# Optimization experiments

Hardware: AMD Instinct MI355X
Metric: run time of the kernel (lower is better)

Reference implementation:

```python
import jax, jax.numpy as jnp
import numpy as np

ATOM_FDIM = 133
BOND_FDIM = 147  # atom features (133) + bond features (14)
HIDDEN = 300
DEPTH = 3
N_ATOMS = 200_000
N_BONDS = 400_000
MAX_NB = 6
N_MOLS = 10_000


def setup_inputs() -> dict:
    key = jax.random.key(0)
    ks = jax.random.split(key, 10)
    f_atoms = jax.random.normal(ks[0], (N_ATOMS, ATOM_FDIM), jnp.float32)
    f_bonds = jax.random.normal(ks[1], (N_BONDS, BOND_FDIM), jnp.float32)
    a2b = jax.random.randint(ks[2], (N_ATOMS, MAX_NB), 0, N_BONDS)
    b2a = jax.random.randint(ks[3], (N_BONDS,), 0, N_ATOMS)
    b2revb = jax.random.randint(ks[4], (N_BONDS,), 0, N_BONDS)
    a2mol = jnp.sort(jax.random.randint(ks[5], (N_ATOMS,), 0, N_MOLS))
    # learned params (chemprop MPNEncoder: W_i/W_h bias=False, W_o bias=True)
    s_i = 1.0 / np.sqrt(BOND_FDIM)
    s_h = 1.0 / np.sqrt(HIDDEN)
    s_o = 1.0 / np.sqrt(ATOM_FDIM + HIDDEN)
    W_i = jax.random.uniform(ks[6], (BOND_FDIM, HIDDEN), jnp.float32, -s_i, s_i)
    W_h = jax.random.uniform(ks[7], (HIDDEN, HIDDEN), jnp.float32, -s_h, s_h)
    W_o = jax.random.uniform(ks[8], (ATOM_FDIM + HIDDEN, HIDDEN), jnp.float32, -s_o, s_o)
    b_o = jax.random.uniform(ks[9], (HIDDEN,), jnp.float32, -s_o, s_o)
    return {"f_atoms": f_atoms, "f_bonds": f_bonds, "W_i": W_i, "W_h": W_h,
            "W_o": W_o, "b_o": b_o, "a2b": a2b, "b2a": b2a, "b2revb": b2revb,
            "a2mol": a2mol, "n_mols": N_MOLS}


def reference(f_atoms, f_bonds, W_i, W_h, W_o, b_o, a2b, b2a, b2revb, a2mol, n_mols):
    # input = W_i(f_bonds); message = ReLU(input)
    inp = f_bonds @ W_i                              # [n_bonds, H]
    message = jax.nn.relu(inp)
    for _ in range(DEPTH - 1):
        # gather incoming bond messages per atom and sum (index_select_ND + sum)
        a_message = message[a2b].sum(axis=1)         # [n_atoms, H]
        # message_b = a_message[b2a] - message[b2revb]
        new_msg = a_message[b2a] - message[b2revb]   # [n_bonds, H]
        message = jax.nn.relu(inp + new_msg @ W_h)
    # final atom hidden states
    a_message = message[a2b].sum(axis=1)             # [n_atoms, H]
    a_input = jnp.concatenate([f_atoms, a_message], axis=1)
    atom_hiddens = jax.nn.relu(a_input @ W_o + b_o)  # [n_atoms, H]
    # mean readout per molecule (scatter-sum / count)
    sums = jax.ops.segment_sum(atom_hiddens, a2mol, num_segments=n_mols)
    counts = jax.ops.segment_sum(jnp.ones((atom_hiddens.shape[0],), atom_hiddens.dtype),
                                 a2mol, num_segments=n_mols)
    mol_vecs = sums / jnp.maximum(counts, 1.0)[:, None]  # [n_mols, H]
    return mol_vecs
```

## Files before the change

### kernel.cpp

```cpp
#include <hip/hip_runtime.h>


#define HID 300
#define AFD 133
#define BFD 147
#define PAD 320

typedef _Float16 h16;
typedef _Float16 f16x8 __attribute__((ext_vector_type(8)));
typedef float    f32x4 __attribute__((ext_vector_type(4)));

__device__ __forceinline__ float relu_(float x) { return x > 0.f ? x : 0.f; }

union FragA { f16x8 v; h16 h[8]; uint4 u4; };
union H4    { uint2 u2; h16 h[4]; };

__global__ __launch_bounds__(256)
void pack_w(const float* __restrict__ Wa, const float* __restrict__ Wb,
            h16* __restrict__ dst, int KT, int mode)
{
    int e = blockIdx.x * 256 + threadIdx.x;
    if (e >= KT * 1280) return;
    int cc = e & 15, g = (e >> 4) & 3, p = (e >> 6) % 20, kt = e / 1280;
    int c = p * 16 + cc;
    FragA w;
    #pragma unroll
    for (int j = 0; j < 8; ++j) {
        int k = kt * 32 + g * 8 + j;
        float x = 0.f;
        if (c < HID) {
            if (mode == 0)      { if (k < BFD) x = Wa[k * HID + c]; }
            else if (mode == 1) { if (k < HID) x = Wa[k * HID + c];
                                  else if (k >= 320 && k < 467) x = Wb[(k - 320) * HID + c]; }
            else                { if (k < AFD) x = Wa[k * HID + c];
                                  else if (k >= 160 && k < 460) x = Wa[(k - 27) * HID + c]; }
        }
        w.h[j] = (h16)x;
    }
    *(uint4*)(dst + (size_t)e * 8) = w.u4;
}

template<int MODE>
__global__ __launch_bounds__(256)
void mgemm(const h16* __restrict__ G, const float* __restrict__ F,
           const h16* __restrict__ Wp, const float* __restrict__ bias,
           h16* __restrict__ outH, float* __restrict__ outF)
{
    constexpr int KT = (MODE == 0) ? 5 : 15;
    const int t  = threadIdx.x;
    const int l  = t & 63, wv = t >> 6;
    const int g  = l >> 4, cc = l & 15;
    const int m0 = blockIdx.x * 64;

    const h16*   pG[4];
    const float* pF[4];
    #pragma unroll
    for (int mt = 0; mt < 4; ++mt) {
        int r = m0 + mt * 16 + cc;
        if (MODE != 0) pG[mt] = G + (size_t)r * PAD + g * 8;
        pF[mt] = F + (size_t)r * ((MODE == 2) ? AFD : BFD);
    }
    const h16* pW = Wp + (size_t)(wv * 5) * 512 + g * 128 + cc * 8;

    f32x4 acc[4][5];
    #pragma unroll
    for (int mt = 0; mt < 4; ++mt)
        #pragma unroll
        for (int nt = 0; nt < 5; ++nt)
            acc[mt][nt] = (f32x4){0.f, 0.f, 0.f, 0.f};

    #pragma unroll
    for (int kt = 0; kt < KT; ++kt) {
        const int ks = kt * 32 + g * 8;
        FragA a[4];
        #pragma unroll
        for (int mt = 0; mt < 4; ++mt) {
            if (MODE == 0) {
                #pragma unroll
                for (int j = 0; j < 8; ++j) {
                    int kk = ks + j;
                    a[mt].h[j] = (h16)((kk < BFD) ? pF[mt][kk] : 0.f);
                }
            } else if (MODE == 1) {
                if (kt < 10) {
                    a[mt].u4 = *(const uint4*)(pG[mt] + kt * 32);
                } else {
                    #pragma unroll
                    for (int j = 0; j < 8; ++j) {
                        int kk = ks - 320 + j;
                        a[mt].h[j] = (h16)((kk < BFD) ? pF[mt][kk] : 0.f);
                    }
                }
            } else {
                if (kt < 5) {
                    #pragma unroll
                    for (int j = 0; j < 8; ++j) {
                        int kk = ks + j;
                        a[mt].h[j] = (h16)((kk < AFD) ? pF[mt][kk] : 0.f);
                    }
                } else {
                    a[mt].u4 = *(const uint4*)(pG[mt] + kt * 32 - 160);
                }
            }
        }
        f16x8 bf[5];
        #pragma unroll
        for (int nt = 0; nt < 5; ++nt)
            bf[nt] = *(const f16x8*)(pW + (size_t)kt * 10240 + nt * 512);
        #pragma unroll
        for (int mt = 0; mt < 4; ++mt)
            #pragma unroll
            for (int nt = 0; nt < 5; ++nt)
                acc[mt][nt] = __builtin_amdgcn_mfma_f32_16x16x32_f16(
                                  a[mt].v, bf[nt], acc[mt][nt], 0, 0, 0);
    }

    #pragma unroll
    for (int mt = 0; mt < 4; ++mt)
        #pragma unroll
        for (int nt = 0; nt < 5; ++nt) {
            int col = (wv * 5 + nt) * 16 + cc;
            float bb = 0.f;
            if (MODE == 2 && col < HID) bb = bias[col];
            #pragma unroll
            for (int rr = 0; rr < 4; ++rr) {
                int row = m0 + mt * 16 + g * 4 + rr;
                float v = relu_(acc[mt][nt][rr] + bb);
                if (MODE == 2) { if (col < HID) outF[(size_t)row * HID + col] = v; }
                else           outH[(size_t)row * PAD + col] = (h16)v;
            }
        }
}

__global__ __launch_bounds__(320)
void gather7(const h16* __restrict__ msg, const int* __restrict__ a2b,
             const int* __restrict__ b2a, const int* __restrict__ b2revb,
             h16* __restrict__ out, int n_bonds)
{
    int gid = blockIdx.x * 320 + threadIdx.x;
    int b = gid / 80, ch = gid - b * 80;
    if (b >= n_bonds) return;
    uint2 o = make_uint2(0u, 0u);
    if (ch < 75) {
        const int* ab = a2b + (size_t)b2a[b] * 6;
        H4 q;
        q.u2 = *(const uint2*)(msg + (size_t)b2revb[b] * PAD + ch * 4);
        float s0 = -(float)q.h[0], s1 = -(float)q.h[1];
        float s2 = -(float)q.h[2], s3 = -(float)q.h[3];
        #pragma unroll
        for (int j = 0; j < 6; ++j) {
            q.u2 = *(const uint2*)(msg + (size_t)ab[j] * PAD + ch * 4);
            s0 += (float)q.h[0]; s1 += (float)q.h[1];
            s2 += (float)q.h[2]; s3 += (float)q.h[3];
        }
        H4 w;
        w.h[0] = (h16)s0; w.h[1] = (h16)s1; w.h[2] = (h16)s2; w.h[3] = (h16)s3;
        o = w.u2;
    }
    *(uint2*)(out + (size_t)b * PAD + ch * 4) = o;
}

__global__ __launch_bounds__(320)
void gather6(const h16* __restrict__ msg, const int* __restrict__ a2b,
             h16* __restrict__ out, int n_atoms)
{
    int gid = blockIdx.x * 320 + threadIdx.x;
    int a = gid / 80, ch = gid - a * 80;
    if (a >= n_atoms) return;
    uint2 o = make_uint2(0u, 0u);
    if (ch < 75) {
        const int* ab = a2b + (size_t)a * 6;
        float s0 = 0.f, s1 = 0.f, s2 = 0.f, s3 = 0.f;
        #pragma unroll
        for (int j = 0; j < 6; ++j) {
            H4 q;
            q.u2 = *(const uint2*)(msg + (size_t)ab[j] * PAD + ch * 4);
            s0 += (float)q.h[0]; s1 += (float)q.h[1];
            s2 += (float)q.h[2]; s3 += (float)q.h[3];
        }
        H4 w;
        w.h[0] = (h16)s0; w.h[1] = (h16)s1; w.h[2] = (h16)s2; w.h[3] = (h16)s3;
        o = w.u2;
    }
    *(uint2*)(out + (size_t)a * PAD + ch * 4) = o;
}

__device__ __forceinline__ int lower_bound_(const int* a, int n, int v)
{
    int lo = 0, hi = n;
    while (lo < hi) { int m = (lo + hi) >> 1; if (a[m] < v) lo = m + 1; else hi = m; }
    return lo;
}

__global__ __launch_bounds__(256)
void mol_mean(const float* __restrict__ hid, const int* __restrict__ a2mol,
              float* __restrict__ out, int n_atoms)
{
    int mol = blockIdx.x;
    int s = lower_bound_(a2mol, n_atoms, mol);
    int e = lower_bound_(a2mol, n_atoms, mol + 1);
    int cnt = e - s;
    float inv = 1.0f / (float)(cnt > 0 ? cnt : 1);
    int t = threadIdx.x;
    float acc0 = 0.f, acc1 = 0.f;
    for (int a = s; a < e; ++a) {
        const float* r = hid + (size_t)a * HID;
        acc0 += r[t];
        if (t < HID - 256) acc1 += r[256 + t];
    }
    out[(size_t)mol * HID + t] = acc0 * inv;
    if (t < HID - 256) out[(size_t)mol * HID + 256 + t] = acc1 * inv;
}

__global__ __launch_bounds__(256)
void sentinel(float* __restrict__ out, int n, float val)
{
    int i = blockIdx.x * 256 + threadIdx.x;
    if (i < n) out[i] = val;
}

extern "C" void kernel_launch(void* const* d_in, const int* in_sizes, int n_in,
                              void* d_out, int out_size, void* d_ws, size_t ws_size,
                              hipStream_t stream)
{
    const float* f_atoms = (const float*)d_in[0];
    const float* f_bonds = (const float*)d_in[1];
    const float* W_i     = (const float*)d_in[2];
    const float* W_h     = (const float*)d_in[3];
    const float* W_o     = (const float*)d_in[4];
    const float* b_o     = (const float*)d_in[5];
    const int*   a2b     = (const int*)d_in[6];
    const int*   b2a     = (const int*)d_in[7];
    const int*   b2revb  = (const int*)d_in[8];
    const int*   a2mol   = (const int*)d_in[9];

    const int n_atoms = in_sizes[0] / AFD;
    const int n_bonds = in_sizes[1] / BFD;
    const int n_mols  = out_size / HID;
    float* out = (float*)d_out;

    const size_t need = (size_t)2 * n_bonds * PAD * sizeof(h16)
                      + (size_t)(5 + 15 + 15) * 1280 * 8 * sizeof(h16);
    if (ws_size < need) {
        float val = (float)(ws_size >> 20) + 0.125f;
        sentinel<<<(out_size + 255) / 256, 256, 0, stream>>>(out, out_size, val);
        return;
    }

    h16* msgA = (h16*)d_ws;
    h16* msgB = msgA + (size_t)n_bonds * PAD;
    h16* Wi_p = msgB + (size_t)n_bonds * PAD;
    h16* Wh_p = Wi_p + (size_t)5  * 1280 * 8;
    h16* Wo_p = Wh_p + (size_t)15 * 1280 * 8;
    h16* amsg = msgB;
    float* hid = (float*)msgA;

    const int gbB = n_bonds / 64;
    const int gbA = n_atoms / 64;
    const int g7  = n_bonds / 4;
    const int g6  = n_atoms / 4;

    pack_w<<<(5 * 1280 + 255) / 256, 256, 0, stream>>>(W_i, nullptr, Wi_p, 5, 0);
    pack_w<<<(15 * 1280 + 255) / 256, 256, 0, stream>>>(W_h, W_i, Wh_p, 15, 1);
    pack_w<<<(15 * 1280 + 255) / 256, 256, 0, stream>>>(W_o, nullptr, Wo_p, 15, 2);

    mgemm<0><<<gbB, 256, 0, stream>>>(nullptr, f_bonds, Wi_p, nullptr, msgA, nullptr);
    gather7<<<g7, 320, 0, stream>>>(msgA, a2b, b2a, b2revb, msgB, n_bonds);
    mgemm<1><<<gbB, 256, 0, stream>>>(msgB, f_bonds, Wh_p, nullptr, msgB, nullptr);
    gather7<<<g7, 320, 0, stream>>>(msgB, a2b, b2a, b2revb, msgA, n_bonds);
    mgemm<1><<<gbB, 256, 0, stream>>>(msgA, f_bonds, Wh_p, nullptr, msgA, nullptr);
    gather6<<<g6, 320, 0, stream>>>(msgA, a2b, amsg, n_atoms);
    mgemm<2><<<gbA, 256, 0, stream>>>(amsg, f_atoms, Wo_p, b_o, nullptr, hid);
    mol_mean<<<n_mols, 256, 0, stream>>>(hid, a2mol, out, n_atoms);
}
```

Before: 2.433 ms.

## Cache fp16 copies of bond/atom features and double-buffer A-fragment loads

The first bond GEMM now writes an fp16 copy of f_bonds, padded to 160 columns, into workspace as it converts them, and a new kernel converts f_atoms to fp16 the same way. Later GEMMs read these copies with 16-byte vector loads instead of doing scalar fp32 loads and converting on every pass. The GEMM main loop also prefetches the next k-tile's A fragments into a second register set, and launch bounds request 3 blocks per SM. This needs extra workspace, so the old path is kept as a fallback. The extra register buffer may hurt occupancy, and the feature copies add one write pass.

```diff
diff --git a/kernel.cpp b/kernel.cpp
--- a/kernel.cpp
+++ b/kernel.cpp
@@ -5,6 +5,7 @@
 #define AFD 133
 #define BFD 147
 #define PAD 320
+#define FBW 160
 
 typedef _Float16 h16;
 typedef _Float16 f16x8 __attribute__((ext_vector_type(8)));
@@ -40,69 +41,87 @@
     *(uint4*)(dst + (size_t)e * 8) = w.u4;
 }
 
-template<int MODE>
 __global__ __launch_bounds__(256)
-void mgemm(const h16* __restrict__ G, const float* __restrict__ F,
-           const h16* __restrict__ Wp, const float* __restrict__ bias,
-           h16* __restrict__ outH, float* __restrict__ outF)
-{
-    constexpr int KT = (MODE == 0) ? 5 : 15;
+void cvt_feat(const float* __restrict__ src, h16* __restrict__ dst,
+              int M, int W, int S)
+{
+    int gid = blockIdx.x * 256 + threadIdx.x;
+    int nchunk = S / 4;
+    int row = gid / nchunk, c4 = (gid % nchunk) * 4;
+    if (row >= M) return;
+    H4 o;
+    #pragma unroll
+    for (int j = 0; j < 4; ++j) {
+        int c = c4 + j;
+        o.h[j] = (h16)((c < W) ? src[(size_t)row * W + c] : 0.f);
+    }
+    *(uint2*)(dst + (size_t)row * S + c4) = o.u2;
+}
+
+template<int MODE, int T16>
+__global__ __launch_bounds__(256, 3)
+void mgemm(const h16* __restrict__ G, const h16* __restrict__ FB,
+           const float* __restrict__ F32, const h16* __restrict__ Wp,
+           const float* __restrict__ bias,
+           h16* __restrict__ outH, float* __restrict__ outF,
+           h16* __restrict__ fbOut)
+{
+    constexpr int KT   = (MODE == 0) ? 5 : 15;
+    constexpr int FW   = (MODE == 2) ? AFD : BFD;
     const int t  = threadIdx.x;
     const int l  = t & 63, wv = t >> 6;
     const int g  = l >> 4, cc = l & 15;
     const int m0 = blockIdx.x * 64;
 
+    int rowv[4];
     const h16*   pG[4];
+    const h16*   pFB[4];
     const float* pF[4];
     #pragma unroll
     for (int mt = 0; mt < 4; ++mt) {
         int r = m0 + mt * 16 + cc;
+        rowv[mt] = r;
         if (MODE != 0) pG[mt] = G + (size_t)r * PAD + g * 8;
-        pF[mt] = F + (size_t)r * ((MODE == 2) ? AFD : BFD);
+        if (T16 && MODE != 0) pFB[mt] = FB + (size_t)r * FBW + g * 8;
+        if (!T16 || MODE == 0) pF[mt] = F32 + (size_t)r * FW;
     }
     const h16* pW = Wp + (size_t)(wv * 5) * 512 + g * 128 + cc * 8;
 
-    f32x4 acc[4][5];
-    #pragma unroll
-    for (int mt = 0; mt < 4; ++mt)
-        #pragma unroll
-        for (int nt = 0; nt < 5; ++nt)
-            acc[mt][nt] = (f32x4){0.f, 0.f, 0.f, 0.f};
-
-    #pragma unroll
-    for (int kt = 0; kt < KT; ++kt) {
-        const int ks = kt * 32 + g * 8;
-        FragA a[4];
-        #pragma unroll
-        for (int mt = 0; mt < 4; ++mt) {
-            if (MODE == 0) {
+    auto loadA = [&](int kt, FragA (&a)[4]) {
+        const bool gReg = (MODE == 1) ? (kt < 10) : (MODE == 2 ? (kt >= 5) : false);
+        if (gReg) {
+            const int off = (MODE == 1) ? kt * 32 : kt * 32 - 160;
+            #pragma unroll
+            for (int mt = 0; mt < 4; ++mt)
+                a[mt].u4 = *(const uint4*)(pG[mt] + off);
+        } else if (T16 && MODE != 0) {
+            const int off = (MODE == 1) ? (kt - 10) * 32 : kt * 32;
+            #pragma unroll
+            for (int mt = 0; mt < 4; ++mt)
+                a[mt].u4 = *(const uint4*)(pFB[mt] + off);
+        } else {
+            const int ks = ((MODE == 1) ? (kt - 10) * 32 : kt * 32) + g * 8;
+            #pragma unroll
+            for (int mt = 0; mt < 4; ++mt) {
                 #pragma unroll
                 for (int j = 0; j < 8; ++j) {
                     int kk = ks + j;
-                    a[mt].h[j] = (h16)((kk < BFD) ? pF[mt][kk] : 0.f);
+                    a[mt].h[j] = (h16)((kk < FW) ? pF[mt][kk] : 0.f);
                 }
-            } else if (MODE == 1) {
-                if (kt < 10) {
-                    a[mt].u4 = *(const uint4*)(pG[mt] + kt * 32);
-                } else {
-                    #pragma unroll
-                    for (int j = 0; j < 8; ++j) {
-                        int kk = ks - 320 + j;
-                        a[mt].h[j] = (h16)((kk < BFD) ? pF[mt][kk] : 0.f);
-                    }
-                }
-            } else {
-                if (kt < 5) {
-                    #pragma unroll
-                    for (int j = 0; j < 8; ++j) {
-                        int kk = ks + j;
-                        a[mt].h[j] = (h16)((kk < AFD) ? pF[mt][kk] : 0.f);
-                    }
-                } else {
-                    a[mt].u4 = *(const uint4*)(pG[mt] + kt * 32 - 160);
-                }
+                if (MODE == 0 && T16)
+                    *(uint4*)(fbOut + (size_t)rowv[mt] * FBW + ks) = a[mt].u4;
             }
         }
+    };
+
+    f32x4 acc[4][5];
+    #pragma unroll
+    for (int mt = 0; mt < 4; ++mt)
+        #pragma unroll
+        for (int nt = 0; nt < 5; ++nt)
+            acc[mt][nt] = (f32x4){0.f, 0.f, 0.f, 0.f};
+
+    auto step = [&](int kt, FragA (&a)[4]) {
         f16x8 bf[5];
         #pragma unroll
         for (int nt = 0; nt < 5; ++nt)
@@ -113,6 +132,19 @@
             for (int nt = 0; nt < 5; ++nt)
                 acc[mt][nt] = __builtin_amdgcn_mfma_f32_16x16x32_f16(
                                   a[mt].v, bf[nt], acc[mt][nt], 0, 0, 0);
+    };
+
+    FragA aX[4], aY[4];
+    loadA(0, aX);
+    #pragma unroll
+    for (int kt = 0; kt < KT; ++kt) {
+        if ((kt & 1) == 0) {
+            if (kt + 1 < KT) loadA(kt + 1, aY);
+            step(kt, aX);
+        } else {
+            if (kt + 1 < KT) loadA(kt + 1, aX);
+            step(kt, aY);
+        }
     }
 
     #pragma unroll
@@ -239,37 +271,70 @@
     const int n_mols  = out_size / HID;
     float* out = (float*)d_out;
 
-    const size_t need = (size_t)2 * n_bonds * PAD * sizeof(h16)
-                      + (size_t)(5 + 15 + 15) * 1280 * 8 * sizeof(h16);
-    if (ws_size < need) {
+    const size_t msgBytes = (size_t)n_bonds * PAD * sizeof(h16);
+    const size_t packByte = (size_t)35 * 1280 * 8 * sizeof(h16);
+    const size_t needT2 = 2 * msgBytes + packByte;
+    const size_t needT1 = needT2 + (size_t)n_bonds * FBW * sizeof(h16)
+                                 + (size_t)n_atoms * FBW * sizeof(h16);
+    const int gbB = n_bonds / 64, gbA = n_atoms / 64;
+    const int g7 = n_bonds / 4, g6 = n_atoms / 4;
+
+    if (ws_size >= needT1) {
+        h16* msgA = (h16*)d_ws;
+        h16* msgB = msgA + (size_t)n_bonds * PAD;
+        h16* fbh  = msgB + (size_t)n_bonds * PAD;
+        h16* fah  = fbh  + (size_t)n_bonds * FBW;
+        h16* Wi_p = fah  + (size_t)n_atoms * FBW;
+        h16* Wh_p = Wi_p + (size_t)5  * 1280 * 8;
+        h16* Wo_p = Wh_p + (size_t)15 * 1280 * 8;
+        h16* amsg = msgB;
+        float* hid = (float*)msgA;
+
+        pack_w<<<(5 * 1280 + 255) / 256, 256, 0, stream>>>(W_i, nullptr, Wi_p, 5, 0);
+        pack_w<<<(15 * 1280 + 255) / 256, 256, 0, stream>>>(W_h, W_i, Wh_p, 15, 1);
+        pack_w<<<(15 * 1280 + 255) / 256, 256, 0, stream>>>(W_o, nullptr, Wo_p, 15, 2);
+        cvt_feat<<<((size_t)n_atoms * (FBW / 4) + 255) / 256, 256, 0, stream>>>(
+            f_atoms, fah, n_atoms, AFD, FBW);
+
+        mgemm<0, 1><<<gbB, 256, 0, stream>>>(nullptr, nullptr, f_bonds, Wi_p,
+                                             nullptr, msgA, nullptr, fbh);
+        gather7<<<g7, 320, 0, stream>>>(msgA, a2b, b2a, b2revb, msgB, n_bonds);
+        mgemm<1, 1><<<gbB, 256, 0, stream>>>(msgB, fbh, nullptr, Wh_p,
+                                             nullptr, msgB, nullptr, nullptr);
+        gather7<<<g7, 320, 0, stream>>>(msgB, a2b, b2a, b2revb, msgA, n_bonds);
+        mgemm<1, 1><<<gbB, 256, 0, stream>>>(msgA, fbh, nullptr, Wh_p,
+                                             nullptr, msgA, nullptr, nullptr);
+        gather6<<<g6, 320, 0, stream>>>(msgA, a2b, amsg, n_atoms);
+        mgemm<2, 1><<<gbA, 256, 0, stream>>>(amsg, fah, nullptr, Wo_p,
+                                             b_o, nullptr, hid, nullptr);
+        mol_mean<<<n_mols, 256, 0, stream>>>(hid, a2mol, out, n_atoms);
+    } else if (ws_size >= needT2) {
+        h16* msgA = (h16*)d_ws;
+        h16* msgB = msgA + (size_t)n_bonds * PAD;
+        h16* Wi_p = msgB + (size_t)n_bonds * PAD;
+        h16* Wh_p = Wi_p + (size_t)5  * 1280 * 8;
+        h16* Wo_p = Wh_p + (size_t)15 * 1280 * 8;
+        h16* amsg = msgB;
+        float* hid = (float*)msgA;
+
+        pack_w<<<(5 * 1280 + 255) / 256, 256, 0, stream>>>(W_i, nullptr, Wi_p, 5, 0);
+        pack_w<<<(15 * 1280 + 255) / 256, 256, 0, stream>>>(W_h, W_i, Wh_p, 15, 1);
+        pack_w<<<(15 * 1280 + 255) / 256, 256, 0, stream>>>(W_o, nullptr, Wo_p, 15, 2);
+
+        mgemm<0, 0><<<gbB, 256, 0, stream>>>(nullptr, nullptr, f_bonds, Wi_p,
+                                             nullptr, msgA, nullptr, nullptr);
+        gather7<<<g7, 320, 0, stream>>>(msgA, a2b, b2a, b2revb, msgB, n_bonds);
+        mgemm<1, 0><<<gbB, 256, 0, stream>>>(msgB, nullptr, f_bonds, Wh_p,
+                                             nullptr, msgB, nullptr, nullptr);
+        gather7<<<g7, 320, 0, stream>>>(msgB, a2b, b2a, b2revb, msgA, n_bonds);
+        mgemm<1, 0><<<gbB, 256, 0, stream>>>(msgA, nullptr, f_bonds, Wh_p,
+                                             nullptr, msgA, nullptr, nullptr);
+        gather6<<<g6, 320, 0, stream>>>(msgA, a2b, amsg, n_atoms);
+        mgemm<2, 0><<<gbA, 256, 0, stream>>>(amsg, nullptr, f_atoms, Wo_p,
+                                             b_o, nullptr, hid, nullptr);
+        mol_mean<<<n_mols, 256, 0, stream>>>(hid, a2mol, out, n_atoms);
+    } else {
         float val = (float)(ws_size >> 20) + 0.125f;
         sentinel<<<(out_size + 255) / 256, 256, 0, stream>>>(out, out_size, val);
-        return;
-    }
-
-    h16* msgA = (h16*)d_ws;
-    h16* msgB = msgA + (size_t)n_bonds * PAD;
-    h16* Wi_p = msgB + (size_t)n_bonds * PAD;
-    h16* Wh_p = Wi_p + (size_t)5  * 1280 * 8;
-    h16* Wo_p = Wh_p + (size_t)15 * 1280 * 8;
-    h16* amsg = msgB;
-    float* hid = (float*)msgA;
-
-    const int gbB = n_bonds / 64;
-    const int gbA = n_atoms / 64;
-    const int g7  = n_bonds / 4;
-    const int g6  = n_atoms / 4;
-
-    pack_w<<<(5 * 1280 + 255) / 256, 256, 0, stream>>>(W_i, nullptr, Wi_p, 5, 0);
-    pack_w<<<(15 * 1280 + 255) / 256, 256, 0, stream>>>(W_h, W_i, Wh_p, 15, 1);
-    pack_w<<<(15 * 1280 + 255) / 256, 256, 0, stream>>>(W_o, nullptr, Wo_p, 15, 2);
-
-    mgemm<0><<<gbB, 256, 0, stream>>>(nullptr, f_bonds, Wi_p, nullptr, msgA, nullptr);
-    gather7<<<g7, 320, 0, stream>>>(msgA, a2b, b2a, b2revb, msgB, n_bonds);
-    mgemm<1><<<gbB, 256, 0, stream>>>(msgB, f_bonds, Wh_p, nullptr, msgB, nullptr);
-    gather7<<<g7, 320, 0, stream>>>(msgB, a2b, b2a, b2revb, msgA, n_bonds);
-    mgemm<1><<<gbB, 256, 0, stream>>>(msgA, f_bonds, Wh_p, nullptr, msgA, nullptr);
-    gather6<<<g6, 320, 0, stream>>>(msgA, a2b, amsg, n_atoms);
-    mgemm<2><<<gbA, 256, 0, stream>>>(amsg, f_atoms, Wo_p, b_o, nullptr, hid);
-    mol_mean<<<n_mols, 256, 0, stream>>>(hid, a2mol, out, n_atoms);
-}
+    }
+}
```

Result: faster. 2.254 ms (-7.4%).
